# Performance work log

Measured on AMD Instinct MI355X. Metric: run time of the kernel, lower is better.

## Reference

```python
import jax, jax.numpy as jnp
import numpy as np

B, C, N, IC = 4, 64, 4096, 32  # batch, in_channels(=g_channels), nodes, inter_channels


def setup_inputs() -> dict:
    key = jax.random.key(0)
    ks = jax.random.split(key, 8)
    s_c = (2.0 / C) ** 0.5   # kaiming-ish scales
    s_i = (2.0 / C) ** 0.5
    x = jax.random.normal(ks[0], (B, C, N), dtype=jnp.float32)
    g_w = jax.random.normal(ks[1], (C, C), dtype=jnp.float32) * s_c      # g: 1x1 conv (out=C, in=C)
    g_b = jnp.zeros((C,), dtype=jnp.float32)
    theta_w = jax.random.normal(ks[2], (IC, C), dtype=jnp.float32) * s_i  # theta: (out=IC, in=C)
    theta_b = jnp.zeros((IC,), dtype=jnp.float32)
    phi_w = jax.random.normal(ks[3], (IC, C), dtype=jnp.float32) * s_i
    phi_b = jnp.zeros((IC,), dtype=jnp.float32)
    cp_w = jax.random.normal(ks[4], (2 * IC,), dtype=jnp.float32) * (2.0 / (2 * IC)) ** 0.5  # concat_project 1x1 conv, no bias
    C_k = jnp.zeros((N, N), dtype=jnp.float32)  # learned adjacency bias, init zeros
    return {"x": x, "g_w": g_w, "g_b": g_b, "theta_w": theta_w, "theta_b": theta_b,
            "phi_w": phi_w, "phi_b": phi_b, "cp_w": cp_w, "C_k": C_k}


def reference(x, g_w, g_b, theta_w, theta_b, phi_w, phi_b, cp_w, C_k):
    # 1x1 convs are plain GEMMs over the node dim
    g_x = jnp.einsum('oc,bcn->bno', g_w, x) + g_b            # (B, N, C)
    th = jnp.einsum('oc,bcn->bon', theta_w, x) + theta_b[:, None]  # (B, IC, N)
    ph = jnp.einsum('oc,bcn->bon', phi_w, x) + phi_b[:, None]      # (B, IC, N)
    # concat_project on [theta_i ; phi_j] with a 1x1 conv is algebraically an outer sum:
    # f[b,i,j] = w_th . theta[b,:,i] + w_ph . phi[b,:,j]
    a = jnp.einsum('c,bcn->bn', cp_w[:IC], th)  # (B, N)
    p = jnp.einsum('c,bcn->bn', cp_w[IC:], ph)  # (B, N)
    f = a[:, :, None] + p[:, None, :]           # (B, N, N)
    attention = jax.nn.softmax(jax.nn.leaky_relu(f, negative_slope=0.2), axis=-1) + C_k
    y = jnp.einsum('bij,bjo->boi', attention, g_x)  # (B, C, N)
    return y
```

## Files before the change

kernel.cpp:

```cpp
#include <hip/hip_runtime.h>


#define B  4
#define C  64
#define N  4096
#define IC 32
#define NS 4104
#define NR 4097
#define MAGIC 0x13572468

#define OFF_FLAG   248
#define OFF_A      256
#define OFF_P      (OFF_A + B*N)
#define OFF_Q      (OFF_P + B*N)
#define OFF_PERM   (OFF_Q + B*N)
#define OFF_PRES   (OFF_PERM + B*N)
#define OFF_SUFS   (OFF_PRES + B*NS)
#define OFF_S1     (OFF_SUFS + B*NS)
#define OFF_S2     (OFF_S1 + B*64*64)
#define OFF_GX     (OFF_S2 + B*64*64)
#define OFF_PREG   (OFF_GX + B*N*64)
#define OFF_SUFG   (OFF_PREG + B*NR*64)

__global__ __launch_bounds__(256) void k1_gx(
    const float* __restrict__ x, const float* __restrict__ g_w,
    const float* __restrict__ g_b, const float* __restrict__ theta_w,
    const float* __restrict__ theta_b, const float* __restrict__ phi_w,
    const float* __restrict__ phi_b, const float* __restrict__ cp_w,
    const float* __restrict__ Ck, float* __restrict__ ws) {
  __shared__ float gwT[C * C];
  __shared__ float xl[C * 16];
  __shared__ float lu[C], lv[C], cst[2];
  const int tid = threadIdx.x;
  const int b = blockIdx.x >> 8;
  const int n0 = (blockIdx.x & 255) << 4;
  for (int idx = tid; idx < C * C; idx += 256) {
    int o = idx >> 6, cc = idx & 63;
    gwT[cc * C + o] = g_w[idx];
  }
  for (int idx = tid; idx < C * 16; idx += 256) {
    int cc = idx >> 4, nn = idx & 15;
    xl[idx] = x[(size_t)((b << 6) + cc) * N + n0 + nn];
  }
  if (tid < 64) {
    float u = 0.f;
    for (int k = 0; k < IC; ++k) u += cp_w[k] * theta_w[k * C + tid];
    lu[tid] = u;
  } else if (tid < 128) {
    int c = tid - 64;
    float v = 0.f;
    for (int k = 0; k < IC; ++k) v += cp_w[IC + k] * phi_w[k * C + c];
    lv[c] = v;
  } else if (tid == 128) {
    float ca = 0.f, cp2 = 0.f;
    for (int k = 0; k < IC; ++k) { ca += cp_w[k] * theta_b[k]; cp2 += cp_w[IC + k] * phi_b[k]; }
    cst[0] = ca; cst[1] = cp2;
  }
  __syncthreads();
  if (tid < 16) {
    float au = cst[0], pu = cst[1];
    for (int cc = 0; cc < C; ++cc) {
      float xv = xl[cc * 16 + tid];
      au += lu[cc] * xv;
      pu += lv[cc] * xv;
    }
    ws[OFF_A + (b << 12) + n0 + tid] = au;
    ws[OFF_P + (b << 12) + n0 + tid] = pu;
  }
  const int o = tid & 63, g4 = tid >> 6;
  float bb = g_b[o];
  float acc0 = bb, acc1 = bb, acc2 = bb, acc3 = bb;
  for (int cc = 0; cc < C; ++cc) {
    float gv = gwT[cc * C + o];
    const float* xr = &xl[cc * 16 + (g4 << 2)];
    acc0 += gv * xr[0]; acc1 += gv * xr[1]; acc2 += gv * xr[2]; acc3 += gv * xr[3];
  }
  float* gx = ws + OFF_GX + (size_t)((b << 12) + n0 + (g4 << 2)) * C + o;
  gx[0] = acc0; gx[64] = acc1; gx[128] = acc2; gx[192] = acc3;
  const float4* c4 = (const float4*)Ck;
  bool nz = false;
  int idx = (blockIdx.x << 8) + tid;
  for (int t = 0; t < 16; ++t) {
    float4 v = c4[idx];
    nz |= (v.x != 0.f) | (v.y != 0.f) | (v.z != 0.f) | (v.w != 0.f);
    idx += 262144;
  }
  if (__any(nz) && (tid & 63) == 0)
    atomicExch((int*)ws + OFF_FLAG, MAGIC);
}

__global__ __launch_bounds__(1024) void k2_rank(float* __restrict__ ws) {
  __shared__ float lp[N];
  __shared__ int partials[32][33];
  const int tid = threadIdx.x;
  const int b = blockIdx.x >> 7;
  const int rg = blockIdx.x & 127;
  const float* p = ws + OFF_P + b * N;
  ((float4*)lp)[tid] = ((const float4*)p)[tid];
  const int row = tid & 31, chunk = tid >> 5;
  const int i = (rg << 5) + row;
  __syncthreads();
  const float my = lp[i];
  const int c0 = chunk << 7;
  const float4* lp4 = (const float4*)(lp + c0);
  int r0 = 0, r1 = 0, r2 = 0, r3 = 0;
  for (int j = 0; j < 32; ++j) {
    float4 v = lp4[j];
    int k = c0 + (j << 2);
    r0 += (v.x < my) || (v.x == my && (k + 0) < i);
    r1 += (v.y < my) || (v.y == my && (k + 1) < i);
    r2 += (v.z < my) || (v.z == my && (k + 2) < i);
    r3 += (v.w < my) || (v.w == my && (k + 3) < i);
  }
  partials[row][chunk] = (r0 + r1) + (r2 + r3);
  __syncthreads();
  if (tid < 32) {
    int rank = 0;
#pragma unroll
    for (int c = 0; c < 32; ++c) rank += partials[tid][c];
    const int ii = (rg << 5) + tid;
    ws[OFF_Q + (b << 12) + rank] = lp[ii];
    ((int*)ws)[OFF_PERM + (b << 12) + rank] = ii;
  }
}

__global__ __launch_bounds__(1024) void k3_scan_chunks(float* __restrict__ ws) {
  __shared__ float sA[1024], sB[1024];
  const int tid = threadIdx.x;
  const int bid = blockIdx.x;
  if (bid < B) {
    const int b = bid;
    float* wt2 = sA;
    float* wt1 = sA + 16;
    float* wo2 = sA + 32;
    float* wo1 = sA + 49;
    const float* q = ws + OFF_Q + b * N;
    const float4 qv4 = ((const float4*)q)[tid];
    float e1r[4], e2r[4];
    e2r[0] = expf(0.2f * qv4.x); e1r[0] = expf(qv4.x);
    e2r[1] = expf(0.2f * qv4.y); e1r[1] = expf(qv4.y);
    e2r[2] = expf(0.2f * qv4.z); e1r[2] = expf(qv4.z);
    e2r[3] = expf(0.2f * qv4.w); e1r[3] = expf(qv4.w);
    float s2 = e2r[0] + e2r[1] + e2r[2] + e2r[3];
    float s1 = e1r[0] + e1r[1] + e1r[2] + e1r[3];
    const int lane = tid & 63, wave = tid >> 6;
    float x2 = s2, x1 = s1;
    for (int off = 1; off < 64; off <<= 1) {
      float t2 = __shfl_up(x2, off, 64);
      float t1 = __shfl_up(x1, off, 64);
      if (lane >= off) { x2 += t2; x1 += t1; }
    }
    if (lane == 63) { wt2[wave] = x2; wt1[wave] = x1; }
    __syncthreads();
    if (wave == 0 && lane < 17) {
      float a2 = 0.f, a1 = 0.f;
      for (int w = 0; w < 16; ++w) {
        if (w < lane) { a2 += wt2[w]; a1 += wt1[w]; }
      }
      wo2[lane] = a2; wo1[lane] = a1;
    }
    __syncthreads();
    const float excl2 = wo2[wave] + (x2 - s2);
    const float incl1 = wo1[wave] + x1;
    const float tot1 = wo1[16];
    float* PreS = ws + OFF_PRES + b * NS;
    float* SufS = ws + OFF_SUFS + b * NS;
    const int base = tid << 2;
    float run = excl2;
#pragma unroll
    for (int j = 0; j < 4; ++j) { PreS[base + j] = run; run += e2r[j]; }
    if (tid == 1023) PreS[N] = run;
    run = tot1 - incl1;
#pragma unroll
    for (int j = 3; j >= 0; --j) { run += e1r[j]; SufS[base + j] = run; }
    if (tid == 1023) SufS[N] = 0.f;
  } else {
    const int b2 = bid - B;
    const int b = b2 >> 6, c = b2 & 63;
    const int o = tid & 63, kk = tid >> 6;
    const float* q = ws + OFF_Q + b * N;
    const int* perm = (const int*)ws + OFF_PERM + b * N;
    const float* gx = ws + OFF_GX + ((size_t)b << 18);
    float p1 = 0.f, p2 = 0.f;
    const int k0 = (c << 6) + (kk << 2);
    for (int r = 0; r < 4; ++r) {
      int k = k0 + r;
      float qv = q[k];
      float g = gx[((size_t)perm[k] << 6) + o];
      p1 += expf(qv) * g;
      p2 += expf(0.2f * qv) * g;
    }
    sA[(kk << 6) + o] = p2;
    sB[(kk << 6) + o] = p1;
    __syncthreads();
    if (tid < 64) {
      float t2 = 0.f, t1 = 0.f;
#pragma unroll
      for (int g = 0; g < 16; ++g) { t2 += sA[(g << 6) + o]; t1 += sB[(g << 6) + o]; }
      ws[OFF_S2 + (size_t)(((b << 6) + c) << 6) + o] = t2;
      ws[OFF_S1 + (size_t)(((b << 6) + c) << 6) + o] = t1;
    }
  }
}

__global__ __launch_bounds__(1024) void k4_prefix(float* __restrict__ ws) {
  __shared__ float sA[1024], sB[1024];
  const int tid = threadIdx.x;
  const int b = blockIdx.x >> 6, c = blockIdx.x & 63;
  const int o = tid & 63, kk = tid >> 6;
  float offp = 0.f, offs = 0.f;
  {
    const float* S1 = ws + OFF_S1 + ((size_t)b << 12);
    const float* S2 = ws + OFF_S2 + ((size_t)b << 12);
    for (int cc = 0; cc < 64; ++cc) {
      float v2 = S2[(cc << 6) + o];
      float v1 = S1[(cc << 6) + o];
      offp += (cc < c) ? v2 : 0.f;
      offs += (cc > c) ? v1 : 0.f;
    }
  }
  const float* q = ws + OFF_Q + b * N;
  const int* perm = (const int*)ws + OFF_PERM + b * N;
  const float* gx = ws + OFF_GX + ((size_t)b << 18);
  float* PreG = ws + OFF_PREG + (size_t)b * NR * 64;
  float* SufG = ws + OFF_SUFG + (size_t)b * NR * 64;
  const int k0 = (c << 6) + (kk << 2);
  float w1[4], w2[4];
  float p1 = 0.f, p2 = 0.f;
  for (int r = 0; r < 4; ++r) {
    float qq = q[k0 + r];
    float gg = gx[((size_t)perm[k0 + r] << 6) + o];
    w1[r] = expf(qq) * gg;
    w2[r] = expf(0.2f * qq) * gg;
    p1 += w1[r]; p2 += w2[r];
  }
  sA[(kk << 6) + o] = p2;
  sB[(kk << 6) + o] = p1;
  __syncthreads();
  for (int kp = 0; kp < kk; ++kp) offp += sA[(kp << 6) + o];
  for (int kp = kk + 1; kp < 16; ++kp) offs += sB[(kp << 6) + o];
  float run = offp;
#pragma unroll
  for (int r = 0; r < 4; ++r) { PreG[(size_t)(k0 + r) * 64 + o] = run; run += w2[r]; }
  if (c == 63 && kk == 15) PreG[(size_t)N * 64 + o] = run;
  run = offs;
#pragma unroll
  for (int r = 3; r >= 0; --r) { run += w1[r]; SufG[(size_t)(k0 + r) * 64 + o] = run; }
  if (c == 0 && kk == 0) SufG[(size_t)N * 64 + o] = 0.f;
}

__global__ __launch_bounds__(1024) void k5_out(const float* __restrict__ Ck,
                                               float* __restrict__ ws,
                                               float* __restrict__ y) {
  __shared__ float lq[N];
  const int tid = threadIdx.x;
  const int b = blockIdx.x >> 6, rg = blockIdx.x & 63;
  const float4* qs = (const float4*)(ws + OFF_Q + b * N);
  ((float4*)lq)[tid] = qs[tid];
  __syncthreads();
  const int io = tid & 63, og = tid >> 6;
  const int i = (rg << 6) + io;
  float ai = ws[OFF_A + (b << 12) + i];
  float thr = -ai;
  int lo = 0, hi = N;
  while (lo < hi) { int m = (lo + hi) >> 1; if (lq[m] <= thr) lo = m + 1; else hi = m; }
  const int k = lo;
  float e1 = expf(ai), e2 = expf(0.2f * ai);
  float den = e1 * ws[OFF_SUFS + b * NS + k] + e2 * ws[OFF_PRES + b * NS + k];
  float inv = 1.0f / den;
  float4 pv = ((const float4*)(ws + OFF_PREG + ((size_t)b * NR + k) * 64))[og];
  float4 sv = ((const float4*)(ws + OFF_SUFG + ((size_t)b * NR + k) * 64))[og];
  float* yb = y + ((size_t)((b << 6) + (og << 2))) * N + i;
  yb[0]             = (e1 * sv.x + e2 * pv.x) * inv;
  yb[(size_t)N]     = (e1 * sv.y + e2 * pv.y) * inv;
  yb[(size_t)2 * N] = (e1 * sv.z + e2 * pv.z) * inv;
  yb[(size_t)3 * N] = (e1 * sv.w + e2 * pv.w) * inv;
  if (((const volatile int*)ws)[OFF_FLAG] == MAGIC) {
    __syncthreads();
    const int it = rg;
    const int o = tid & 63, jj = tid >> 6;
    const float* gx = ws + OFF_GX + ((size_t)b << 18);
    float (*red)[64] = (float(*)[64])lq;
    for (int ii = 0; ii < 64; ++ii) {
      int irow = (it << 6) + ii;
      float acc = 0.f;
      for (int j = jj; j < N; j += 16)
        acc += Ck[(size_t)irow * N + j] * gx[((size_t)j << 6) + o];
      red[jj][o] = acc;
      __syncthreads();
      if (jj == 0) {
        float s = 0.f;
#pragma unroll
        for (int g = 0; g < 16; ++g) s += red[g][o];
        y[((size_t)((b << 6) + o)) * N + irow] += s;
      }
      __syncthreads();
    }
  }
}

extern "C" void kernel_launch(void* const* d_in, const int* in_sizes, int n_in,
                              void* d_out, int out_size, void* d_ws, size_t ws_size,
                              hipStream_t stream) {
  (void)in_sizes; (void)n_in; (void)out_size; (void)ws_size;
  const float* x       = (const float*)d_in[0];
  const float* g_w     = (const float*)d_in[1];
  const float* g_b     = (const float*)d_in[2];
  const float* theta_w = (const float*)d_in[3];
  const float* theta_b = (const float*)d_in[4];
  const float* phi_w   = (const float*)d_in[5];
  const float* phi_b   = (const float*)d_in[6];
  const float* cp_w    = (const float*)d_in[7];
  const float* Ck      = (const float*)d_in[8];
  float* ws = (float*)d_ws;
  float* y  = (float*)d_out;

  hipLaunchKernelGGL(k1_gx, dim3(1024), dim3(256), 0, stream,
                     x, g_w, g_b, theta_w, theta_b, phi_w, phi_b, cp_w, Ck, ws);
  hipLaunchKernelGGL(k2_rank, dim3(512), dim3(1024), 0, stream, ws);
  hipLaunchKernelGGL(k3_scan_chunks, dim3(B + B * 64), dim3(1024), 0, stream, ws);
  hipLaunchKernelGGL(k4_prefix, dim3(B * 64), dim3(1024), 0, stream, ws);
  hipLaunchKernelGGL(k5_out, dim3(B * 64), dim3(1024), 0, stream, Ck, ws, y);
}
```

Before: 149.8 us.

## Fuse rank, chunk-scan and output kernels into one cooperative kernel with grid barriers

Merges the rank, scan, prefix and output kernels into a single cooperative kernel of 256 blocks separated by hierarchical atomic grid barriers. The full per-position prefix/suffix arrays (PreG/SufG, PreS/SufS) are no longer written. Instead each output row uses per-chunk prefix offsets plus a direct 64-element partial sum inside its chunk. This removes launch overhead and most of the large prefix-array memory traffic, at the cost of spin-barrier latency and some extra exp/gather work per output.

```diff
diff --git a/kernel.cpp b/kernel.cpp
--- a/kernel.cpp
+++ b/kernel.cpp
@@ -5,22 +5,20 @@
 #define C  64
 #define N  4096
 #define IC 32
-#define NS 4104
-#define NR 4097
 #define MAGIC 0x13572468
+#define NBLK 256
 
 #define OFF_FLAG   248
 #define OFF_A      256
 #define OFF_P      (OFF_A + B*N)
 #define OFF_Q      (OFF_P + B*N)
 #define OFF_PERM   (OFF_Q + B*N)
-#define OFF_PRES   (OFF_PERM + B*N)
-#define OFF_SUFS   (OFF_PRES + B*NS)
-#define OFF_S1     (OFF_SUFS + B*NS)
+#define OFF_S1     (OFF_PERM + B*N)
 #define OFF_S2     (OFF_S1 + B*64*64)
-#define OFF_GX     (OFF_S2 + B*64*64)
-#define OFF_PREG   (OFF_GX + B*N*64)
-#define OFF_SUFG   (OFF_PREG + B*NR*64)
+#define OFF_SC1    (OFF_S2 + B*64*64)
+#define OFF_SC2    (OFF_SC1 + B*64)
+#define OFF_BAR    (OFF_SC2 + B*64)
+#define OFF_GX     (OFF_BAR + 2048)
 
 __global__ __launch_bounds__(256) void k1_gx(
     const float* __restrict__ x, const float* __restrict__ g_w,
@@ -34,6 +32,9 @@
   const int tid = threadIdx.x;
   const int b = blockIdx.x >> 8;
   const int n0 = (blockIdx.x & 255) << 4;
+  if (blockIdx.x == 0) {
+    for (int j = tid; j < 1088; j += 256) ((int*)ws)[OFF_BAR + j] = 0;
+  }
   for (int idx = tid; idx < C * C; idx += 256) {
     int o = idx >> 6, cc = idx & 63;
     gwT[cc * C + o] = g_w[idx];
@@ -89,209 +90,183 @@
     atomicExch((int*)ws + OFF_FLAG, MAGIC);
 }
 
-__global__ __launch_bounds__(1024) void k2_rank(float* __restrict__ ws) {
-  __shared__ float lp[N];
-  __shared__ int partials[32][33];
-  const int tid = threadIdx.x;
-  const int b = blockIdx.x >> 7;
-  const int rg = blockIdx.x & 127;
-  const float* p = ws + OFF_P + b * N;
-  ((float4*)lp)[tid] = ((const float4*)p)[tid];
-  const int row = tid & 31, chunk = tid >> 5;
-  const int i = (rg << 5) + row;
+__device__ __forceinline__ void gridbar(int* bar, int slot) {
   __syncthreads();
-  const float my = lp[i];
-  const int c0 = chunk << 7;
-  const float4* lp4 = (const float4*)(lp + c0);
-  int r0 = 0, r1 = 0, r2 = 0, r3 = 0;
-  for (int j = 0; j < 32; ++j) {
-    float4 v = lp4[j];
-    int k = c0 + (j << 2);
-    r0 += (v.x < my) || (v.x == my && (k + 0) < i);
-    r1 += (v.y < my) || (v.y == my && (k + 1) < i);
-    r2 += (v.z < my) || (v.z == my && (k + 2) < i);
-    r3 += (v.w < my) || (v.w == my && (k + 3) < i);
-  }
-  partials[row][chunk] = (r0 + r1) + (r2 + r3);
+  if (threadIdx.x == 0) {
+    __threadfence();
+    int* base = bar + slot * 544;
+    int* g    = base + (blockIdx.x & 15) * 32;
+    int* root = base + 512;
+    if (__hip_atomic_fetch_add(g, 1, __ATOMIC_RELAXED,
+                               __HIP_MEMORY_SCOPE_AGENT) == 15)
+      __hip_atomic_fetch_add(root, 1, __ATOMIC_RELAXED,
+                             __HIP_MEMORY_SCOPE_AGENT);
+    while (__hip_atomic_load(root, __ATOMIC_RELAXED,
+                             __HIP_MEMORY_SCOPE_AGENT) < 16) {
+      __builtin_amdgcn_s_sleep(1);
+    }
+    __threadfence();
+  }
   __syncthreads();
-  if (tid < 32) {
-    int rank = 0;
-#pragma unroll
-    for (int c = 0; c < 32; ++c) rank += partials[tid][c];
-    const int ii = (rg << 5) + tid;
-    ws[OFF_Q + (b << 12) + rank] = lp[ii];
-    ((int*)ws)[OFF_PERM + (b << 12) + rank] = ii;
-  }
-}
-
-__global__ __launch_bounds__(1024) void k3_scan_chunks(float* __restrict__ ws) {
-  __shared__ float sA[1024], sB[1024];
+}
+
+__global__ __launch_bounds__(1024) void fused(const float* __restrict__ Ck,
+                                              float* __restrict__ ws,
+                                              float* __restrict__ y) {
+  __shared__ float smem[12416];
   const int tid = threadIdx.x;
   const int bid = blockIdx.x;
-  if (bid < B) {
-    const int b = bid;
-    float* wt2 = sA;
-    float* wt1 = sA + 16;
-    float* wo2 = sA + 32;
-    float* wo1 = sA + 49;
-    const float* q = ws + OFF_Q + b * N;
-    const float4 qv4 = ((const float4*)q)[tid];
-    float e1r[4], e2r[4];
-    e2r[0] = expf(0.2f * qv4.x); e1r[0] = expf(qv4.x);
-    e2r[1] = expf(0.2f * qv4.y); e1r[1] = expf(qv4.y);
-    e2r[2] = expf(0.2f * qv4.z); e1r[2] = expf(qv4.z);
-    e2r[3] = expf(0.2f * qv4.w); e1r[3] = expf(qv4.w);
-    float s2 = e2r[0] + e2r[1] + e2r[2] + e2r[3];
-    float s1 = e1r[0] + e1r[1] + e1r[2] + e1r[3];
-    const int lane = tid & 63, wave = tid >> 6;
-    float x2 = s2, x1 = s1;
-    for (int off = 1; off < 64; off <<= 1) {
-      float t2 = __shfl_up(x2, off, 64);
-      float t1 = __shfl_up(x1, off, 64);
-      if (lane >= off) { x2 += t2; x1 += t1; }
-    }
-    if (lane == 63) { wt2[wave] = x2; wt1[wave] = x1; }
-    __syncthreads();
-    if (wave == 0 && lane < 17) {
-      float a2 = 0.f, a1 = 0.f;
-      for (int w = 0; w < 16; ++w) {
-        if (w < lane) { a2 += wt2[w]; a1 += wt1[w]; }
-      }
-      wo2[lane] = a2; wo1[lane] = a1;
-    }
-    __syncthreads();
-    const float excl2 = wo2[wave] + (x2 - s2);
-    const float incl1 = wo1[wave] + x1;
-    const float tot1 = wo1[16];
-    float* PreS = ws + OFF_PRES + b * NS;
-    float* SufS = ws + OFF_SUFS + b * NS;
-    const int base = tid << 2;
-    float run = excl2;
-#pragma unroll
-    for (int j = 0; j < 4; ++j) { PreS[base + j] = run; run += e2r[j]; }
-    if (tid == 1023) PreS[N] = run;
-    run = tot1 - incl1;
-#pragma unroll
-    for (int j = 3; j >= 0; --j) { run += e1r[j]; SufS[base + j] = run; }
-    if (tid == 1023) SufS[N] = 0.f;
-  } else {
-    const int b2 = bid - B;
-    const int b = b2 >> 6, c = b2 & 63;
+  int* bar = (int*)ws + OFF_BAR;
+  const int b  = bid >> 6;
+  const int rg = bid & 63;
+
+  {
+    float* lp = smem;
+    int* partials = (int*)(smem + 4096);
+    const float* p = ws + OFF_P + b * N;
+    ((float4*)lp)[tid] = ((const float4*)p)[tid];
+    const int row = tid & 63, chunk = tid >> 6;
+    const int i = (rg << 6) + row;
+    __syncthreads();
+    const float my = lp[i];
+    const int c0 = chunk << 8;
+    const float4* lp4 = (const float4*)(lp + c0);
+    int r0 = 0, r1 = 0, r2 = 0, r3 = 0;
+    for (int j = 0; j < 64; ++j) {
+      float4 v = lp4[j];
+      int k = c0 + (j << 2);
+      r0 += (v.x < my) || (v.x == my && (k + 0) < i);
+      r1 += (v.y < my) || (v.y == my && (k + 1) < i);
+      r2 += (v.z < my) || (v.z == my && (k + 2) < i);
+      r3 += (v.w < my) || (v.w == my && (k + 3) < i);
+    }
+    partials[row * 17 + chunk] = (r0 + r1) + (r2 + r3);
+    __syncthreads();
+    if (tid < 64) {
+      int rank = 0;
+#pragma unroll
+      for (int c2 = 0; c2 < 16; ++c2) rank += partials[tid * 17 + c2];
+      const int ii = (rg << 6) + tid;
+      ws[OFF_Q + (b << 12) + rank] = lp[ii];
+      ((int*)ws)[OFF_PERM + (b << 12) + rank] = ii;
+    }
+  }
+  gridbar(bar, 0);
+
+  {
+    const int c = rg;
     const int o = tid & 63, kk = tid >> 6;
     const float* q = ws + OFF_Q + b * N;
     const int* perm = (const int*)ws + OFF_PERM + b * N;
     const float* gx = ws + OFF_GX + ((size_t)b << 18);
-    float p1 = 0.f, p2 = 0.f;
+    float p1 = 0.f, p2 = 0.f, se1 = 0.f, se2 = 0.f;
     const int k0 = (c << 6) + (kk << 2);
     for (int r = 0; r < 4; ++r) {
       int k = k0 + r;
       float qv = q[k];
+      float e1v = expf(qv), e2v = expf(0.2f * qv);
       float g = gx[((size_t)perm[k] << 6) + o];
-      p1 += expf(qv) * g;
-      p2 += expf(0.2f * qv) * g;
-    }
+      p1 += e1v * g; p2 += e2v * g;
+      se1 += e1v; se2 += e2v;
+    }
+    float* sA = smem; float* sB = smem + 1024;
+    float* ss1 = smem + 2048; float* ss2 = smem + 2064;
     sA[(kk << 6) + o] = p2;
     sB[(kk << 6) + o] = p1;
+    if (o == 0) { ss1[kk] = se1; ss2[kk] = se2; }
     __syncthreads();
     if (tid < 64) {
       float t2 = 0.f, t1 = 0.f;
 #pragma unroll
-      for (int g = 0; g < 16; ++g) { t2 += sA[(g << 6) + o]; t1 += sB[(g << 6) + o]; }
+      for (int g2 = 0; g2 < 16; ++g2) { t2 += sA[(g2 << 6) + o]; t1 += sB[(g2 << 6) + o]; }
       ws[OFF_S2 + (size_t)(((b << 6) + c) << 6) + o] = t2;
       ws[OFF_S1 + (size_t)(((b << 6) + c) << 6) + o] = t1;
-    }
-  }
-}
-
-__global__ __launch_bounds__(1024) void k4_prefix(float* __restrict__ ws) {
-  __shared__ float sA[1024], sB[1024];
-  const int tid = threadIdx.x;
-  const int b = blockIdx.x >> 6, c = blockIdx.x & 63;
-  const int o = tid & 63, kk = tid >> 6;
-  float offp = 0.f, offs = 0.f;
+    } else if (tid == 64) {
+      float t1 = 0.f, t2 = 0.f;
+#pragma unroll
+      for (int g2 = 0; g2 < 16; ++g2) { t1 += ss1[g2]; t2 += ss2[g2]; }
+      ws[OFF_SC1 + (b << 6) + c] = t1;
+      ws[OFF_SC2 + (b << 6) + c] = t2;
+    }
+  }
+  gridbar(bar, 1);
+
   {
-    const float* S1 = ws + OFF_S1 + ((size_t)b << 12);
-    const float* S2 = ws + OFF_S2 + ((size_t)b << 12);
-    for (int cc = 0; cc < 64; ++cc) {
-      float v2 = S2[(cc << 6) + o];
-      float v1 = S1[(cc << 6) + o];
-      offp += (cc < c) ? v2 : 0.f;
-      offs += (cc > c) ? v1 : 0.f;
-    }
-  }
-  const float* q = ws + OFF_Q + b * N;
-  const int* perm = (const int*)ws + OFF_PERM + b * N;
-  const float* gx = ws + OFF_GX + ((size_t)b << 18);
-  float* PreG = ws + OFF_PREG + (size_t)b * NR * 64;
-  float* SufG = ws + OFF_SUFG + (size_t)b * NR * 64;
-  const int k0 = (c << 6) + (kk << 2);
-  float w1[4], w2[4];
-  float p1 = 0.f, p2 = 0.f;
-  for (int r = 0; r < 4; ++r) {
-    float qq = q[k0 + r];
-    float gg = gx[((size_t)perm[k0 + r] << 6) + o];
-    w1[r] = expf(qq) * gg;
-    w2[r] = expf(0.2f * qq) * gg;
-    p1 += w1[r]; p2 += w2[r];
-  }
-  sA[(kk << 6) + o] = p2;
-  sB[(kk << 6) + o] = p1;
-  __syncthreads();
-  for (int kp = 0; kp < kk; ++kp) offp += sA[(kp << 6) + o];
-  for (int kp = kk + 1; kp < 16; ++kp) offs += sB[(kp << 6) + o];
-  float run = offp;
-#pragma unroll
-  for (int r = 0; r < 4; ++r) { PreG[(size_t)(k0 + r) * 64 + o] = run; run += w2[r]; }
-  if (c == 63 && kk == 15) PreG[(size_t)N * 64 + o] = run;
-  run = offs;
-#pragma unroll
-  for (int r = 3; r >= 0; --r) { run += w1[r]; SufG[(size_t)(k0 + r) * 64 + o] = run; }
-  if (c == 0 && kk == 0) SufG[(size_t)N * 64 + o] = 0.f;
-}
-
-__global__ __launch_bounds__(1024) void k5_out(const float* __restrict__ Ck,
-                                               float* __restrict__ ws,
-                                               float* __restrict__ y) {
-  __shared__ float lq[N];
-  const int tid = threadIdx.x;
-  const int b = blockIdx.x >> 6, rg = blockIdx.x & 63;
-  const float4* qs = (const float4*)(ws + OFF_Q + b * N);
-  ((float4*)lq)[tid] = qs[tid];
-  __syncthreads();
-  const int io = tid & 63, og = tid >> 6;
-  const int i = (rg << 6) + io;
-  float ai = ws[OFF_A + (b << 12) + i];
-  float thr = -ai;
-  int lo = 0, hi = N;
-  while (lo < hi) { int m = (lo + hi) >> 1; if (lq[m] <= thr) lo = m + 1; else hi = m; }
-  const int k = lo;
-  float e1 = expf(ai), e2 = expf(0.2f * ai);
-  float den = e1 * ws[OFF_SUFS + b * NS + k] + e2 * ws[OFF_PRES + b * NS + k];
-  float inv = 1.0f / den;
-  float4 pv = ((const float4*)(ws + OFF_PREG + ((size_t)b * NR + k) * 64))[og];
-  float4 sv = ((const float4*)(ws + OFF_SUFG + ((size_t)b * NR + k) * 64))[og];
-  float* yb = y + ((size_t)((b << 6) + (og << 2))) * N + i;
-  yb[0]             = (e1 * sv.x + e2 * pv.x) * inv;
-  yb[(size_t)N]     = (e1 * sv.y + e2 * pv.y) * inv;
-  yb[(size_t)2 * N] = (e1 * sv.z + e2 * pv.z) * inv;
-  yb[(size_t)3 * N] = (e1 * sv.w + e2 * pv.w) * inv;
+    float* lq    = smem;
+    float* offP  = smem + 4096;
+    float* offS  = smem + 8192;
+    float* offPS = smem + 12288;
+    float* offSS = smem + 12352;
+    ((float4*)lq)[tid] = ((const float4*)(ws + OFF_Q + b * N))[tid];
+    if (tid < 64) {
+      const float* S2g = ws + OFF_S2 + ((size_t)b << 12);
+      float run = 0.f;
+      for (int c2 = 0; c2 < 64; ++c2) { offP[(c2 << 6) + tid] = run; run += S2g[(c2 << 6) + tid]; }
+    } else if (tid < 128) {
+      const int o = tid - 64;
+      const float* S1g = ws + OFF_S1 + ((size_t)b << 12);
+      float run = 0.f;
+      for (int c2 = 63; c2 >= 0; --c2) { offS[(c2 << 6) + o] = run; run += S1g[(c2 << 6) + o]; }
+    } else if (tid == 128) {
+      const float* sc2 = ws + OFF_SC2 + (b << 6);
+      float run = 0.f;
+      for (int c2 = 0; c2 < 64; ++c2) { offPS[c2] = run; run += sc2[c2]; }
+    } else if (tid == 129) {
+      const float* sc1 = ws + OFF_SC1 + (b << 6);
+      float run = 0.f;
+      for (int c2 = 63; c2 >= 0; --c2) { offSS[c2] = run; run += sc1[c2]; }
+    }
+    __syncthreads();
+    const int io = tid & 63, og = tid >> 6;
+    const int i = (rg << 6) + io;
+    const float ai = ws[OFF_A + (b << 12) + i];
+    const float thr = -ai;
+    int lo = 0, hi = N;
+    while (lo < hi) { int m = (lo + hi) >> 1; if (lq[m] <= thr) lo = m + 1; else hi = m; }
+    const int k = lo;
+    const int ce = min(k >> 6, 63);
+    const int j0 = ce << 6;
+    const float e1 = expf(ai), e2 = expf(0.2f * ai);
+    const int* perm = (const int*)ws + OFF_PERM + b * N;
+    const float* gxb = ws + OFF_GX + ((size_t)b << 18) + (og << 2);
+    float4 acc = {0.f, 0.f, 0.f, 0.f};
+    float ds = 0.f;
+    for (int j = j0; j < j0 + 64; ++j) {
+      float t = ai + lq[j];
+      float targ = (j < k) ? 0.2f * t : t;
+      float w = expf(targ);
+      int pj = perm[j];
+      const float4 g4 = *(const float4*)(gxb + ((size_t)pj << 6));
+      acc.x += w * g4.x; acc.y += w * g4.y; acc.z += w * g4.z; acc.w += w * g4.w;
+      ds += w;
+    }
+    float den = e1 * offSS[ce] + e2 * offPS[ce] + ds;
+    float inv = 1.0f / den;
+    float4 op4 = *(float4*)(offP + (ce << 6) + (og << 2));
+    float4 os4 = *(float4*)(offS + (ce << 6) + (og << 2));
+    float* yb = y + ((size_t)((b << 6) + (og << 2))) * N + i;
+    yb[0]             = (e1 * os4.x + e2 * op4.x + acc.x) * inv;
+    yb[(size_t)N]     = (e1 * os4.y + e2 * op4.y + acc.y) * inv;
+    yb[(size_t)2 * N] = (e1 * os4.z + e2 * op4.z + acc.z) * inv;
+    yb[(size_t)3 * N] = (e1 * os4.w + e2 * op4.w + acc.w) * inv;
+  }
+
   if (((const volatile int*)ws)[OFF_FLAG] == MAGIC) {
     __syncthreads();
-    const int it = rg;
     const int o = tid & 63, jj = tid >> 6;
     const float* gx = ws + OFF_GX + ((size_t)b << 18);
-    float (*red)[64] = (float(*)[64])lq;
+    float (*red)[64] = (float(*)[64])smem;
     for (int ii = 0; ii < 64; ++ii) {
-      int irow = (it << 6) + ii;
-      float acc = 0.f;
+      int irow = (rg << 6) + ii;
+      float acc2 = 0.f;
       for (int j = jj; j < N; j += 16)
-        acc += Ck[(size_t)irow * N + j] * gx[((size_t)j << 6) + o];
-      red[jj][o] = acc;
+        acc2 += Ck[(size_t)irow * N + j] * gx[((size_t)j << 6) + o];
+      red[jj][o] = acc2;
       __syncthreads();
       if (jj == 0) {
         float s = 0.f;
 #pragma unroll
-        for (int g = 0; g < 16; ++g) s += red[g][o];
+        for (int g2 = 0; g2 < 16; ++g2) s += red[g2][o];
         y[((size_t)((b << 6) + o)) * N + irow] += s;
       }
       __syncthreads();
@@ -317,8 +292,7 @@
 
   hipLaunchKernelGGL(k1_gx, dim3(1024), dim3(256), 0, stream,
                      x, g_w, g_b, theta_w, theta_b, phi_w, phi_b, cp_w, Ck, ws);
-  hipLaunchKernelGGL(k2_rank, dim3(512), dim3(1024), 0, stream, ws);
-  hipLaunchKernelGGL(k3_scan_chunks, dim3(B + B * 64), dim3(1024), 0, stream, ws);
-  hipLaunchKernelGGL(k4_prefix, dim3(B * 64), dim3(1024), 0, stream, ws);
-  hipLaunchKernelGGL(k5_out, dim3(B * 64), dim3(1024), 0, stream, Ck, ws, y);
-}
+  void* args[] = {(void*)&Ck, (void*)&ws, (void*)&y};
+  hipLaunchCooperativeKernel((const void*)fused, dim3(NBLK), dim3(1024), args,
+                             0, stream);
+}
```

After: 227.4 us. 51.9% more time.

## Drop full prefix/suffix scan kernel; compute in-chunk partial sums in output kernel

Applied to the files above, without the earlier changes.

Removes the separate prefix kernel that wrote full per-position prefix and suffix arrays of weighted g_x. The sums kernel now writes the weighted terms per sorted position, and the output kernel rebuilds chunk offsets from the per-chunk sums in shared memory. Each output row then adds up to 64 entries within its chunk to form the numerator. This saves one launch and the recomputation of the weighted terms, but adds a per-row strided read loop in the output kernel. Output is now staged through shared memory so the stores to y are coalesced.

```diff
diff --git a/kernel.cpp b/kernel.cpp
--- a/kernel.cpp
+++ b/kernel.cpp
@@ -6,7 +6,6 @@
 #define N  4096
 #define IC 32
 #define NS 4104
-#define NR 4097
 #define MAGIC 0x13572468
 
 #define OFF_FLAG   248
@@ -19,8 +18,8 @@
 #define OFF_S1     (OFF_SUFS + B*NS)
 #define OFF_S2     (OFF_S1 + B*64*64)
 #define OFF_GX     (OFF_S2 + B*64*64)
-#define OFF_PREG   (OFF_GX + B*N*64)
-#define OFF_SUFG   (OFF_PREG + B*NR*64)
+#define OFF_GS1    (OFF_GX + B*N*64)
+#define OFF_GS2    (OFF_GS1 + B*N*64)
 
 __global__ __launch_bounds__(256) void k1_gx(
     const float* __restrict__ x, const float* __restrict__ g_w,
@@ -124,12 +123,42 @@
   }
 }
 
-__global__ __launch_bounds__(1024) void k3_scan_chunks(float* __restrict__ ws) {
+__global__ __launch_bounds__(1024) void k3_sums(float* __restrict__ ws) {
   __shared__ float sA[1024], sB[1024];
   const int tid = threadIdx.x;
   const int bid = blockIdx.x;
-  if (bid < B) {
-    const int b = bid;
+  if (bid < B * 64) {
+    const int b = bid >> 6, c = bid & 63;
+    const int o = tid & 63, kk = tid >> 6;
+    const float* q = ws + OFF_Q + b * N;
+    const int* perm = (const int*)ws + OFF_PERM + b * N;
+    const float* gx = ws + OFF_GX + ((size_t)b << 18);
+    float* gs1 = ws + OFF_GS1 + ((size_t)b << 18);
+    float* gs2 = ws + OFF_GS2 + ((size_t)b << 18);
+    float p1 = 0.f, p2 = 0.f;
+    const int k0 = (c << 6) + (kk << 2);
+    for (int r = 0; r < 4; ++r) {
+      int k = k0 + r;
+      float qv = q[k];
+      float e1v = expf(qv), e2v = expf(0.2f * qv);
+      float g = gx[((size_t)perm[k] << 6) + o];
+      float w1 = e1v * g, w2 = e2v * g;
+      gs1[((size_t)k << 6) + o] = w1;
+      gs2[((size_t)k << 6) + o] = w2;
+      p1 += w1; p2 += w2;
+    }
+    sA[(kk << 6) + o] = p2;
+    sB[(kk << 6) + o] = p1;
+    __syncthreads();
+    if (tid < 64) {
+      float t2 = 0.f, t1 = 0.f;
+#pragma unroll
+      for (int g2 = 0; g2 < 16; ++g2) { t2 += sA[(g2 << 6) + o]; t1 += sB[(g2 << 6) + o]; }
+      ws[OFF_S2 + (size_t)(((b << 6) + c) << 6) + o] = t2;
+      ws[OFF_S1 + (size_t)(((b << 6) + c) << 6) + o] = t1;
+    }
+  } else {
+    const int b = bid - B * 64;
     float* wt2 = sA;
     float* wt1 = sA + 16;
     float* wo2 = sA + 32;
@@ -174,124 +203,107 @@
 #pragma unroll
     for (int j = 3; j >= 0; --j) { run += e1r[j]; SufS[base + j] = run; }
     if (tid == 1023) SufS[N] = 0.f;
-  } else {
-    const int b2 = bid - B;
-    const int b = b2 >> 6, c = b2 & 63;
-    const int o = tid & 63, kk = tid >> 6;
-    const float* q = ws + OFF_Q + b * N;
-    const int* perm = (const int*)ws + OFF_PERM + b * N;
-    const float* gx = ws + OFF_GX + ((size_t)b << 18);
-    float p1 = 0.f, p2 = 0.f;
-    const int k0 = (c << 6) + (kk << 2);
-    for (int r = 0; r < 4; ++r) {
-      int k = k0 + r;
-      float qv = q[k];
-      float g = gx[((size_t)perm[k] << 6) + o];
-      p1 += expf(qv) * g;
-      p2 += expf(0.2f * qv) * g;
-    }
-    sA[(kk << 6) + o] = p2;
-    sB[(kk << 6) + o] = p1;
-    __syncthreads();
-    if (tid < 64) {
-      float t2 = 0.f, t1 = 0.f;
-#pragma unroll
-      for (int g = 0; g < 16; ++g) { t2 += sA[(g << 6) + o]; t1 += sB[(g << 6) + o]; }
-      ws[OFF_S2 + (size_t)(((b << 6) + c) << 6) + o] = t2;
-      ws[OFF_S1 + (size_t)(((b << 6) + c) << 6) + o] = t1;
-    }
-  }
-}
-
-__global__ __launch_bounds__(1024) void k4_prefix(float* __restrict__ ws) {
-  __shared__ float sA[1024], sB[1024];
-  const int tid = threadIdx.x;
-  const int b = blockIdx.x >> 6, c = blockIdx.x & 63;
-  const int o = tid & 63, kk = tid >> 6;
-  float offp = 0.f, offs = 0.f;
-  {
-    const float* S1 = ws + OFF_S1 + ((size_t)b << 12);
-    const float* S2 = ws + OFF_S2 + ((size_t)b << 12);
-    for (int cc = 0; cc < 64; ++cc) {
-      float v2 = S2[(cc << 6) + o];
-      float v1 = S1[(cc << 6) + o];
-      offp += (cc < c) ? v2 : 0.f;
-      offs += (cc > c) ? v1 : 0.f;
-    }
-  }
-  const float* q = ws + OFF_Q + b * N;
-  const int* perm = (const int*)ws + OFF_PERM + b * N;
-  const float* gx = ws + OFF_GX + ((size_t)b << 18);
-  float* PreG = ws + OFF_PREG + (size_t)b * NR * 64;
-  float* SufG = ws + OFF_SUFG + (size_t)b * NR * 64;
-  const int k0 = (c << 6) + (kk << 2);
-  float w1[4], w2[4];
-  float p1 = 0.f, p2 = 0.f;
-  for (int r = 0; r < 4; ++r) {
-    float qq = q[k0 + r];
-    float gg = gx[((size_t)perm[k0 + r] << 6) + o];
-    w1[r] = expf(qq) * gg;
-    w2[r] = expf(0.2f * qq) * gg;
-    p1 += w1[r]; p2 += w2[r];
-  }
-  sA[(kk << 6) + o] = p2;
-  sB[(kk << 6) + o] = p1;
-  __syncthreads();
-  for (int kp = 0; kp < kk; ++kp) offp += sA[(kp << 6) + o];
-  for (int kp = kk + 1; kp < 16; ++kp) offs += sB[(kp << 6) + o];
-  float run = offp;
-#pragma unroll
-  for (int r = 0; r < 4; ++r) { PreG[(size_t)(k0 + r) * 64 + o] = run; run += w2[r]; }
-  if (c == 63 && kk == 15) PreG[(size_t)N * 64 + o] = run;
-  run = offs;
-#pragma unroll
-  for (int r = 3; r >= 0; --r) { run += w1[r]; SufG[(size_t)(k0 + r) * 64 + o] = run; }
-  if (c == 0 && kk == 0) SufG[(size_t)N * 64 + o] = 0.f;
-}
-
-__global__ __launch_bounds__(1024) void k5_out(const float* __restrict__ Ck,
+  }
+}
+
+__global__ __launch_bounds__(1024) void k4_out(const float* __restrict__ Ck,
                                                float* __restrict__ ws,
                                                float* __restrict__ y) {
-  __shared__ float lq[N];
+  __shared__ float lqy[4224];
+  __shared__ float offP[4096];
+  __shared__ float offS[4096];
   const int tid = threadIdx.x;
   const int b = blockIdx.x >> 6, rg = blockIdx.x & 63;
-  const float4* qs = (const float4*)(ws + OFF_Q + b * N);
-  ((float4*)lq)[tid] = qs[tid];
-  __syncthreads();
-  const int io = tid & 63, og = tid >> 6;
-  const int i = (rg << 6) + io;
-  float ai = ws[OFF_A + (b << 12) + i];
-  float thr = -ai;
-  int lo = 0, hi = N;
-  while (lo < hi) { int m = (lo + hi) >> 1; if (lq[m] <= thr) lo = m + 1; else hi = m; }
-  const int k = lo;
-  float e1 = expf(ai), e2 = expf(0.2f * ai);
-  float den = e1 * ws[OFF_SUFS + b * NS + k] + e2 * ws[OFF_PRES + b * NS + k];
-  float inv = 1.0f / den;
-  float4 pv = ((const float4*)(ws + OFF_PREG + ((size_t)b * NR + k) * 64))[og];
-  float4 sv = ((const float4*)(ws + OFF_SUFG + ((size_t)b * NR + k) * 64))[og];
-  float* yb = y + ((size_t)((b << 6) + (og << 2))) * N + i;
-  yb[0]             = (e1 * sv.x + e2 * pv.x) * inv;
-  yb[(size_t)N]     = (e1 * sv.y + e2 * pv.y) * inv;
-  yb[(size_t)2 * N] = (e1 * sv.z + e2 * pv.z) * inv;
-  yb[(size_t)3 * N] = (e1 * sv.w + e2 * pv.w) * inv;
+  float* lq = lqy;
+  ((float4*)lq)[tid] = ((const float4*)(ws + OFF_Q + b * N))[tid];
+  if (tid < 64) {
+    const float* S2g = ws + OFF_S2 + ((size_t)b << 12);
+    float run = 0.f;
+    for (int c2 = 0; c2 < 64; ++c2) { offP[(c2 << 6) + tid] = run; run += S2g[(c2 << 6) + tid]; }
+  } else if (tid < 128) {
+    const int o = tid - 64;
+    const float* S1g = ws + OFF_S1 + ((size_t)b << 12);
+    float run = 0.f;
+    for (int c2 = 63; c2 >= 0; --c2) { offS[(c2 << 6) + o] = run; run += S1g[(c2 << 6) + o]; }
+  }
+  __syncthreads();
+  const int wave = tid >> 6, lane = tid & 63;
+  int r_k[4], r_ce[4];
+  float r_e1[4], r_e2[4], r_inv[4];
+#pragma unroll
+  for (int rr = 0; rr < 4; ++rr) {
+    const int row = (wave << 2) + rr;
+    const int i = (rg << 6) + row;
+    const float ai = ws[OFF_A + (b << 12) + i];
+    const float thr = -ai;
+    int lo = 0, hi = N;
+    while (lo < hi) { int m = (lo + hi) >> 1; if (lq[m] <= thr) lo = m + 1; else hi = m; }
+    r_k[rr] = lo;
+    r_ce[rr] = min(lo >> 6, 63);
+    r_e1[rr] = expf(ai);
+    r_e2[rr] = expf(0.2f * ai);
+    float den = r_e1[rr] * ws[OFF_SUFS + b * NS + lo] +
+                r_e2[rr] * ws[OFF_PRES + b * NS + lo];
+    r_inv[rr] = 1.0f / den;
+  }
+  __syncthreads();
+  float* yblk = lqy;
+  const float* gs1 = ws + OFF_GS1 + ((size_t)b << 18) + lane;
+  const float* gs2 = ws + OFF_GS2 + ((size_t)b << 18) + lane;
+#pragma unroll
+  for (int rr = 0; rr < 4; ++rr) {
+    const int row = (wave << 2) + rr;
+    const int ce = r_ce[rr], j0 = ce << 6, m = r_k[rr] - j0;
+    const float* g2p = gs2 + ((size_t)j0 << 6);
+    const float* g1p = gs1 + ((size_t)j0 << 6);
+    float a0 = 0.f, a1 = 0.f, a2 = 0.f, a3 = 0.f;
+    float b0 = 0.f, b1 = 0.f, b2 = 0.f, b3 = 0.f;
+    int j = 0;
+    for (; j + 4 <= m; j += 4) {
+      a0 += g2p[(size_t)(j + 0) << 6];
+      a1 += g2p[(size_t)(j + 1) << 6];
+      a2 += g2p[(size_t)(j + 2) << 6];
+      a3 += g2p[(size_t)(j + 3) << 6];
+    }
+    for (; j < m; ++j) a0 += g2p[(size_t)j << 6];
+    for (; j + 4 <= 64; j += 4) {
+      b0 += g1p[(size_t)(j + 0) << 6];
+      b1 += g1p[(size_t)(j + 1) << 6];
+      b2 += g1p[(size_t)(j + 2) << 6];
+      b3 += g1p[(size_t)(j + 3) << 6];
+    }
+    for (; j < 64; ++j) b0 += g1p[(size_t)j << 6];
+    float accA = (a0 + a1) + (a2 + a3);
+    float accB = (b0 + b1) + (b2 + b3);
+    float num = r_e1[rr] * (offS[(ce << 6) + lane] + accB) +
+                r_e2[rr] * (offP[(ce << 6) + lane] + accA);
+    yblk[row * 65 + lane] = num * r_inv[rr];
+  }
+  __syncthreads();
+  {
+    const int i = lane, o0 = wave << 2;
+#pragma unroll
+    for (int rr = 0; rr < 4; ++rr) {
+      int o = o0 + rr;
+      y[((size_t)((b << 6) + o)) * N + (rg << 6) + i] = yblk[i * 65 + o];
+    }
+  }
   if (((const volatile int*)ws)[OFF_FLAG] == MAGIC) {
     __syncthreads();
-    const int it = rg;
     const int o = tid & 63, jj = tid >> 6;
-    const float* gx = ws + OFF_GX + ((size_t)b << 18);
-    float (*red)[64] = (float(*)[64])lq;
+    const float* gxb = ws + OFF_GX + ((size_t)b << 18);
+    float (*red)[64] = (float(*)[64])lqy;
     for (int ii = 0; ii < 64; ++ii) {
-      int irow = (it << 6) + ii;
-      float acc = 0.f;
+      int irow = (rg << 6) + ii;
+      float acc2 = 0.f;
       for (int j = jj; j < N; j += 16)
-        acc += Ck[(size_t)irow * N + j] * gx[((size_t)j << 6) + o];
-      red[jj][o] = acc;
+        acc2 += Ck[(size_t)irow * N + j] * gxb[((size_t)j << 6) + o];
+      red[jj][o] = acc2;
       __syncthreads();
       if (jj == 0) {
         float s = 0.f;
 #pragma unroll
-        for (int g = 0; g < 16; ++g) s += red[g][o];
+        for (int g2 = 0; g2 < 16; ++g2) s += red[g2][o];
         y[((size_t)((b << 6) + o)) * N + irow] += s;
       }
       __syncthreads();
@@ -318,7 +330,6 @@
   hipLaunchKernelGGL(k1_gx, dim3(1024), dim3(256), 0, stream,
                      x, g_w, g_b, theta_w, theta_b, phi_w, phi_b, cp_w, Ck, ws);
   hipLaunchKernelGGL(k2_rank, dim3(512), dim3(1024), 0, stream, ws);
-  hipLaunchKernelGGL(k3_scan_chunks, dim3(B + B * 64), dim3(1024), 0, stream, ws);
-  hipLaunchKernelGGL(k4_prefix, dim3(B * 64), dim3(1024), 0, stream, ws);
-  hipLaunchKernelGGL(k5_out, dim3(B * 64), dim3(1024), 0, stream, Ck, ws, y);
-}
+  hipLaunchKernelGGL(k3_sums, dim3(B * 64 + B), dim3(1024), 0, stream, ws);
+  hipLaunchKernelGGL(k4_out, dim3(B * 64), dim3(1024), 0, stream, Ck, ws, y);
+}
```

New measurement: 170.2 us. +13.6%, slower.
